# Kernel tuning notes

Hardware: AMD Instinct MI355X
Metric: run time of the kernel (lower is better)

Reference implementation:

```python
import jax, jax.numpy as jnp
import numpy as np

B, D, CIN, H, W = 2, 6, 3, 96, 96
DIM, NUM_HEADS, DEPTH = 144, 6, 2
WS = (2, 8, 8)   # window size (d, h, w)
SS = (1, 4, 4)   # shift size for odd blocks
HID = int(DIM * 2.0)
TBL = (2 * WS[0] - 1) * (2 * WS[1] - 1) * (2 * WS[2] - 1)  # 675
EPS = 1e-5


def _rpi(ws):
    # pairwise relative position index, same math as WindowAttention.get_position_index
    coords = np.stack(np.meshgrid(np.arange(ws[0]), np.arange(ws[1]), np.arange(ws[2]), indexing='ij'))
    cf = coords.reshape(3, -1).astype(np.int64)
    rc = (cf[:, :, None] - cf[:, None, :]).transpose(1, 2, 0)
    rc[..., 0] += ws[0] - 1
    rc[..., 1] += ws[1] - 1
    rc[..., 2] += ws[2] - 1
    rc[..., 0] *= (2 * ws[1] - 1) * (2 * ws[2] - 1)
    rc[..., 1] *= 2 * ws[2] - 1
    return rc.sum(-1)  # (N, N)


def _win_part_np(x, ws):
    b, d, h, w, c = x.shape
    x = x.reshape(b, d // ws[0], ws[0], h // ws[1], ws[1], w // ws[2], ws[2], c)
    return x.transpose(0, 1, 3, 5, 2, 4, 6, 7).reshape(-1, ws[0] * ws[1] * ws[2], c)


def _attn_mask(Dp, Hp, Wp, ws, ss):
    # static shift-window attention mask, same as compute_mask
    img = np.zeros((1, Dp, Hp, Wp, 1), np.float32)
    cnt = 0
    for d in (slice(-ws[0]), slice(-ws[0], -ss[0]), slice(-ss[0], None)):
        for h in (slice(-ws[1]), slice(-ws[1], -ss[1]), slice(-ss[1], None)):
            for w in (slice(-ws[2]), slice(-ws[2], -ss[2]), slice(-ss[2], None)):
                img[:, d, h, w, :] = cnt
                cnt += 1
    mw = _win_part_np(img, ws)[..., 0]  # (nW, N)
    am = mw[:, None, :] - mw[:, :, None]
    return np.where(am != 0, np.float32(-100.0), np.float32(0.0))


RPI = jnp.asarray(_rpi(WS))            # (N, N) int
MASK = jnp.asarray(_attn_mask(D, H, W, WS, SS))  # (nW, N, N)


def _ln(x, g, b):
    mu = jnp.mean(x, -1, keepdims=True)
    var = jnp.mean(jnp.square(x - mu), -1, keepdims=True)
    return (x - mu) * jax.lax.rsqrt(var + EPS) * g + b


def _win_part(x, ws):
    b, d, h, w, c = x.shape
    x = x.reshape(b, d // ws[0], ws[0], h // ws[1], ws[1], w // ws[2], ws[2], c)
    return x.transpose(0, 1, 3, 5, 2, 4, 6, 7).reshape(-1, ws[0] * ws[1] * ws[2], c)


def _win_rev(xw, ws, b, d, h, w):
    x = xw.reshape(b, d // ws[0], h // ws[1], w // ws[2], ws[0], ws[1], ws[2], -1)
    return x.transpose(0, 1, 4, 2, 5, 3, 6, 7).reshape(b, d, h, w, -1)


def _stl(x, i, shifted, params):
    # one Swin Transformer Layer; x: (B, D, H, W, C)
    n1g, n1b, qkvw, qkvb, rpb, projw, projb, n2g, n2b, fc1w, fc1b, fc2w, fc2b = params
    b, d, h, w, c = x.shape
    hd = c // NUM_HEADS
    scale = hd ** -0.5
    y = _ln(x, n1g[i], n1b[i])
    if shifted:
        y = jnp.roll(y, (-SS[0], -SS[1], -SS[2]), axis=(1, 2, 3))
    xw = _win_part(y, WS)  # (B_, N, C)
    B_, N, _ = xw.shape
    qkv = jnp.einsum('bnc,oc->bno', xw, qkvw[i]) + qkvb[i]
    qkv = qkv.reshape(B_, N, 3, NUM_HEADS, hd).transpose(2, 0, 3, 1, 4)
    q, k, v = qkv[0], qkv[1], qkv[2]
    attn = jnp.einsum('bhnd,bhmd->bhnm', q * scale, k)
    bias = rpb[i][RPI].transpose(2, 0, 1)  # (heads, N, N)
    attn = attn + bias[None]
    if shifted:
        nW = MASK.shape[0]
        attn = attn.reshape(B_ // nW, nW, NUM_HEADS, N, N) + MASK[None, :, None]
        attn = attn.reshape(B_, NUM_HEADS, N, N)
    attn = jax.nn.softmax(attn, axis=-1)
    out = jnp.einsum('bhnm,bhmd->bhnd', attn, v).transpose(0, 2, 1, 3).reshape(B_, N, c)
    out = jnp.einsum('bnc,oc->bno', out, projw[i]) + projb[i]
    y = _win_rev(out, WS, b, d, h, w)
    if shifted:
        y = jnp.roll(y, (SS[0], SS[1], SS[2]), axis=(1, 2, 3))
    x = x + y
    z = _ln(x, n2g[i], n2b[i])
    z = jnp.einsum('bdhwc,oc->bdhwo', z, fc1w[i]) + fc1b[i]
    z = jax.nn.gelu(z, approximate=False)
    z = jnp.einsum('bdhwo,co->bdhwc', z, fc2w[i]) + fc2b[i]
    return x + z


def setup_inputs() -> dict:
    key = jax.random.key(0)
    ks = jax.random.split(key, 8)
    s = 0.02
    return {
        'x': jax.random.normal(ks[0], (B, D, CIN, H, W), jnp.float32),
        'conv_w': jax.random.normal(ks[1], (DIM, CIN, 1, 3, 3), jnp.float32) * s,
        'conv_b': jnp.zeros((DIM,), jnp.float32),
        'ln0_g': jnp.ones((DIM,), jnp.float32),
        'ln0_b': jnp.zeros((DIM,), jnp.float32),
        'n1g': jnp.ones((DEPTH, DIM), jnp.float32),
        'n1b': jnp.zeros((DEPTH, DIM), jnp.float32),
        'qkvw': jax.random.normal(ks[2], (DEPTH, 3 * DIM, DIM), jnp.float32) * s,
        'qkvb': jnp.zeros((DEPTH, 3 * DIM), jnp.float32),
        'rpb': jax.random.normal(ks[3], (DEPTH, TBL, NUM_HEADS), jnp.float32) * s,
        'projw': jax.random.normal(ks[4], (DEPTH, DIM, DIM), jnp.float32) * s,
        'projb': jnp.zeros((DEPTH, DIM), jnp.float32),
        'n2g': jnp.ones((DEPTH, DIM), jnp.float32),
        'n2b': jnp.zeros((DEPTH, DIM), jnp.float32),
        'fc1w': jax.random.normal(ks[5], (DEPTH, HID, DIM), jnp.float32) * s,
        'fc1b': jnp.zeros((DEPTH, HID), jnp.float32),
        'fc2w': jax.random.normal(ks[6], (DEPTH, DIM, HID), jnp.float32) * s,
        'fc2b': jnp.zeros((DEPTH, DIM), jnp.float32),
        'lin_w': jax.random.normal(ks[7], (DIM, DIM), jnp.float32) * s,
        'lin_b': jnp.zeros((DIM,), jnp.float32),
        'ln1_g': jnp.ones((DIM,), jnp.float32),
        'ln1_b': jnp.zeros((DIM,), jnp.float32),
    }


def reference(x, conv_w, conv_b, ln0_g, ln0_b, n1g, n1b, qkvw, qkvb, rpb, projw, projb,
              n2g, n2b, fc1w, fc1b, fc2w, fc2b, lin_w, lin_b, ln1_g, ln1_b):
    # x: (n, d, c, h, w)
    y = x.transpose(0, 2, 1, 3, 4)  # n c d h w
    y = jax.lax.conv_general_dilated(
        y, conv_w, (1, 1, 1), [(0, 0), (1, 1), (1, 1)],
        dimension_numbers=('NCDHW', 'OIDHW', 'NCDHW')) + conv_b[None, :, None, None, None]
    y = y.transpose(0, 2, 3, 4, 1)  # n d h w c
    y = _ln(y, ln0_g, ln0_b)
    y = y.transpose(0, 4, 1, 2, 3)  # n c d h w
    params = (n1g, n1b, qkvw, qkvb, rpb, projw, projb, n2g, n2b, fc1w, fc1b, fc2w, fc2b)
    # RSTB (num_blocks = 1): residual group (STG of DEPTH STLs) + linear + skip
    f = y.transpose(0, 2, 3, 4, 1)  # b d h w c
    for i in range(DEPTH):
        f = _stl(f, i, i % 2 == 1, params)
    f = jnp.einsum('bdhwc,oc->bdhwo', f, lin_w) + lin_b
    y = y + f.transpose(0, 4, 1, 2, 3)
    # trailing LayerNorm and rearrange back to (n, d, c, h, w)
    out = _ln(y.transpose(0, 2, 3, 4, 1), ln1_g, ln1_b)
    return out.transpose(0, 1, 4, 2, 3)
```

## Files before the change

### kernel.cpp

```cpp
#include <hip/hip_runtime.h>
#include <math.h>

#define NTOK 110592
#define NWIN 864
#define TS   15925248

typedef unsigned short u16;
typedef unsigned int   u32;
typedef __attribute__((ext_vector_type(8))) short short8;
typedef __attribute__((ext_vector_type(4))) float float4v;

__device__ __forceinline__ float bf2f(u16 v) { return __uint_as_float(((u32)v) << 16); }
__device__ __forceinline__ u16 f2bf(float f) {
    u32 u = __float_as_uint(f);
    u32 r = u + 0x7fffu + ((u >> 16) & 1u);
    return (u16)(r >> 16);
}
__device__ __forceinline__ void unpack2(u32 u, float& lo, float& hi) {
    lo = __uint_as_float(u << 16);
    hi = __uint_as_float(u & 0xffff0000u);
}
__device__ __forceinline__ u32 pack2(float lo, float hi) {
    return (u32)f2bf(lo) | ((u32)f2bf(hi) << 16);
}
__device__ __forceinline__ float wave_sum(float v) {
    #pragma unroll
    for (int o = 32; o > 0; o >>= 1) v += __shfl_xor(v, o, 64);
    return v;
}
__device__ __forceinline__ float fexp2(float x) {
    float r;
    asm("v_exp_f32 %0, %1" : "=v"(r) : "v"(x));
    return r;
}

__device__ __forceinline__ void win_to_src(int tw, int shifted, int& sb, int& sd, int& sh, int& sw) {
    int n = tw & 127;
    int win = tw >> 7;
    int ww = win % 12;
    int wh = (win / 12) % 12;
    int rest = win / 144;
    int wd = rest % 3;
    sb = rest / 3;
    int ld = n >> 6, lh = (n >> 3) & 7, lw = n & 7;
    int dr = wd * 2 + ld, hr = wh * 8 + lh, wr = ww * 8 + lw;
    if (shifted) {
        sd = (dr + 1) % 6;
        sh = (hr + 4) % 96;
        sw = (wr + 4) % 96;
    } else {
        sd = dr; sh = hr; sw = wr;
    }
}

__device__ __forceinline__ int tok_region(int t, int wdn, int whn, int wwn) {
    int dr = wdn * 2 + (t >> 6), hr = whn * 8 + ((t >> 3) & 7), wr = wwn * 8 + (t & 7);
    int rd = (dr < 4) ? 0 : ((dr < 5) ? 1 : 2);
    int rh = (hr < 88) ? 0 : ((hr < 92) ? 1 : 2);
    int rw = (wr < 88) ? 0 : ((wr < 92) ? 1 : 2);
    return rd * 9 + rh * 3 + rw;
}

__global__ __launch_bounds__(256) void convert_weights(
    const float* __restrict__ qkvw, const float* __restrict__ projw,
    const float* __restrict__ fc1w, const float* __restrict__ fc2w,
    const float* __restrict__ linw, u16* __restrict__ wbuf,
    const float* __restrict__ rpb, float* __restrict__ bexp)
{
    int i = blockIdx.x * 256 + threadIdx.x;
    if (i < 124416) wbuf[i] = f2bf(qkvw[i]);
    else if (i < 165888) wbuf[i] = f2bf(projw[i - 124416]);
    else if (i < 248832) wbuf[i] = f2bf(fc1w[i - 165888]);
    else if (i < 331776) wbuf[i] = f2bf(fc2w[i - 248832]);
    else if (i < 352512) wbuf[i] = f2bf(linw[i - 331776]);
    else if (i < 549120) {
        int k = i - 352512;
        int n = k & 127, m = (k >> 7) & 127;
        int lh = k >> 14;
        int h = lh % 6, l = lh / 6;
        int rdi = (m >> 6) - (n >> 6) + 1;
        int rhi = ((m >> 3) & 7) - ((n >> 3) & 7) + 7;
        int rwi = (m & 7) - (n & 7) + 7;
        int bi = (rdi * 15 + rhi) * 15 + rwi;
        bexp[k] = rpb[l * 4050 + bi * 6 + h] * 1.4426950408889634f;
    }
}

__global__ __launch_bounds__(256) void conv_ln0_row(
    const float* __restrict__ x, const float* __restrict__ cw, const float* __restrict__ cb,
    const float* __restrict__ g0, const float* __restrict__ b0,
    float* __restrict__ y0)
{
    int bh = blockIdx.x;
    int h = bh % 96, bd = bh / 96;
    int b = bd / 6, d = bd - b * 6;
    __shared__ float ws[192][29];
    __shared__ float xsr[9][100];
    __shared__ float cbias[192], gg[144], bbv[144];
    int tid = threadIdx.x;

    for (int i = tid; i < 9 * 98; i += 256) {
        int row = i / 98, wx = i - row * 98;
        int ci = row / 3, kh = row - 3 * ci;
        int hh = h + kh - 1, wsrc = wx - 1;
        float v = 0.f;
        if (hh >= 0 && hh < 96 && wsrc >= 0 && wsrc < 96)
            v = x[((((size_t)b * 6 + d) * 3 + ci) * 96 + hh) * 96 + wsrc];
        xsr[row][wx] = v;
    }
    for (int i = tid; i < 192 * 27; i += 256) {
        int c = i / 27, j = i - c * 27;
        ws[c][j] = (c < 144) ? cw[c * 27 + j] : 0.f;
    }
    for (int i = tid; i < 192; i += 256) cbias[i] = (i < 144) ? cb[i] : 0.f;
    for (int i = tid; i < 144; i += 256) { gg[i] = g0[i]; bbv[i] = b0[i]; }
    __syncthreads();

    int wv = tid >> 6, lane = tid & 63;
    int p0 = wv * 24;

    float a0[24], a1[24], a2[24];
    #pragma unroll
    for (int k = 0; k < 24; k++) {
        a0[k] = cbias[lane]; a1[k] = cbias[lane + 64]; a2[k] = cbias[lane + 128];
    }

    for (int cikh = 0; cikh < 9; cikh++) {
        const float* xr = &xsr[cikh][p0];
        float xv[26];
        #pragma unroll
        for (int t = 0; t < 26; t++) xv[t] = xr[t];
        #pragma unroll
        for (int kw = 0; kw < 3; kw++) {
            int j = cikh * 3 + kw;
            float w0 = ws[lane][j], w1 = ws[lane + 64][j], w2 = ws[lane + 128][j];
            #pragma unroll
            for (int k = 0; k < 24; k++) {
                float xvv = xv[k + kw];
                a0[k] += w0 * xvv; a1[k] += w1 * xvv; a2[k] += w2 * xvv;
            }
        }
    }

    #pragma unroll
    for (int k = 0; k < 24; k++) {
        int p = p0 + k;
        float v0 = a0[k], v1 = a1[k];
        float v2m = (lane < 16) ? a2[k] : 0.f;
        float s  = wave_sum(v0 + v1 + v2m);
        float s2 = wave_sum(v0 * v0 + v1 * v1 + v2m * v2m);
        float mu = s * (1.f / 144.f);
        float rstd = rsqrtf(fmaxf(s2 * (1.f / 144.f) - mu * mu, 0.f) + 1e-5f);
        size_t o = ((size_t)bh * 96 + p) * 144;
        float r0 = (v0 - mu) * rstd * gg[lane] + bbv[lane];
        float r1 = (v1 - mu) * rstd * gg[lane + 64] + bbv[lane + 64];
        y0[o + lane] = r0;
        y0[o + lane + 64] = r1;
        if (lane < 16) {
            float r2 = (a2[k] - mu) * rstd * gg[lane + 128] + bbv[lane + 128];
            y0[o + lane + 128] = r2;
        }
    }
}

template<int AMODE, int EPI, int SHIFTED, int ADDBIAS, int KTILES>
__global__ __launch_bounds__(192) void mgemm(
    const void* __restrict__ Asrc, const u16* __restrict__ Wt, const float* __restrict__ bias,
    u16* __restrict__ outb, float* __restrict__ fres, const float* __restrict__ y0,
    const float* __restrict__ lng, const float* __restrict__ lnb,
    int a_add, int a_ld, int w_ld, int o_ld, int o_add)
{
    __shared__ u16 As[64 * 152];
    int m0 = blockIdx.y * 64, n0 = blockIdx.x * 144;
    int tid = threadIdx.x;
    int wv3 = tid / 64, lane = tid & 63;
    int mrow = lane & 15, quad = lane >> 4;
    const short8 z8 = {0, 0, 0, 0, 0, 0, 0, 0};

    float4v acc[4][3];
    #pragma unroll
    for (int i = 0; i < 4; i++)
        #pragma unroll
        for (int j = 0; j < 3; j++) acc[i][j] = (float4v){0.f, 0.f, 0.f, 0.f};

    #pragma unroll
    for (int kt = 0; kt < KTILES; kt++) {
        if (kt) __syncthreads();
        if constexpr (AMODE == 5 || AMODE == 6) {
            __shared__ float gs[144], bs[144], ps[64][6];
            for (int i = tid; i < 144; i += 192) { gs[i] = lng[i]; bs[i] = lnb[i]; }
            int r = tid / 3, p = tid - 3 * r;
            int srow;
            if constexpr (AMODE == 6) {
                int bq, dq, hq, wq;
                win_to_src(a_add + m0 + r, SHIFTED, bq, dq, hq, wq);
                srow = ((bq * 6 + dq) * 96 + hq) * 96 + wq;
            } else {
                srow = a_add + m0 + r;
            }
            const float4* s4 = (const float4*)((const float*)Asrc + (size_t)srow * 144) + p * 12;
            float4 av[12];
            float s = 0.f, s2 = 0.f;
            #pragma unroll
            for (int q = 0; q < 12; q++) {
                av[q] = s4[q];
                s  += (av[q].x + av[q].y) + (av[q].z + av[q].w);
                s2 += (av[q].x * av[q].x + av[q].y * av[q].y)
                    + (av[q].z * av[q].z + av[q].w * av[q].w);
            }
            ps[r][p] = s; ps[r][3 + p] = s2;
            __syncthreads();
            float S  = ps[r][0] + ps[r][1] + ps[r][2];
            float S2 = ps[r][3] + ps[r][4] + ps[r][5];
            float mu = S * (1.f / 144.f);
            float rstd = rsqrtf(fmaxf(S2 * (1.f / 144.f) - mu * mu, 0.f) + 1e-5f);
            #pragma unroll
            for (int q = 0; q < 12; q++) {
                int n = p * 48 + q * 4;
                *(u32*)&As[r * 152 + n]     = pack2((av[q].x - mu) * rstd * gs[n]     + bs[n],
                                                    (av[q].y - mu) * rstd * gs[n + 1] + bs[n + 1]);
                *(u32*)&As[r * 152 + n + 2] = pack2((av[q].z - mu) * rstd * gs[n + 2] + bs[n + 2],
                                                    (av[q].w - mu) * rstd * gs[n + 3] + bs[n + 3]);
            }
        } else if constexpr (AMODE == 2) {
            const u16* A = (const u16*)Asrc;
            #pragma unroll
            for (int idx = tid; idx < 1152; idx += 192) {
                int r = idx / 18, c4 = idx - r * 18;
                *(short8*)&As[r * 152 + c4 * 8] =
                    *(const short8*)&A[(size_t)(a_add + m0 + r) * a_ld + kt * 144 + c4 * 8];
            }
        } else if constexpr (AMODE == 3) {
            const u16* A = (const u16*)Asrc;
            int chtok = a_ld;
            int cc = m0 / chtok;
            int t0 = m0 - cc * chtok;
            const u16* Ac = A + (size_t)cc * chtok * 144;
            #pragma unroll
            for (int idx = tid; idx < 1152; idx += 192) {
                int r = idx / 18, c4 = idx - r * 18;
                int hh = c4 / 3, sub = c4 - hh * 3;
                *(short8*)&As[r * 152 + c4 * 8] =
                    *(const short8*)&Ac[((size_t)hh * chtok + t0 + r) * 24 + sub * 8];
            }
        } else {
            const float* A = (const float*)Asrc;
            #pragma unroll
            for (int idx = tid; idx < 2304; idx += 192) {
                int r = idx / 36, c4 = idx - r * 36;
                const float4* src4 = (const float4*)&A[(size_t)(a_add + m0 + r) * a_ld + kt * 144];
                float4 v = src4[c4];
                *(u32*)&As[r * 152 + c4 * 4]     = pack2(v.x, v.y);
                *(u32*)&As[r * 152 + c4 * 4 + 2] = pack2(v.z, v.w);
            }
        }
        __syncthreads();

        const u16* Wg = Wt + (size_t)(n0 + wv3 * 48 + mrow) * w_ld + kt * 144;

        #pragma unroll
        for (int ks = 0; ks < 4; ks++) {
            int k0 = ks * 32;
            short8 af[4], bf[3];
            #pragma unroll
            for (int i = 0; i < 4; i++)
                af[i] = *(const short8*)&As[(i * 16 + mrow) * 152 + k0 + quad * 8];
            #pragma unroll
            for (int j = 0; j < 3; j++)
                bf[j] = *(const short8*)&Wg[(size_t)j * 16 * w_ld + k0 + quad * 8];
            #pragma unroll
            for (int i = 0; i < 4; i++)
                #pragma unroll
                for (int j = 0; j < 3; j++)
                    acc[i][j] = __builtin_amdgcn_mfma_f32_16x16x32_bf16(af[i], bf[j], acc[i][j], 0, 0, 0);
        }
        {
            bool tl = (quad < 2);
            short8 af[4], bf[3];
            #pragma unroll
            for (int i = 0; i < 4; i++)
                af[i] = tl ? *(const short8*)&As[(i * 16 + mrow) * 152 + 128 + quad * 8] : z8;
            #pragma unroll
            for (int j = 0; j < 3; j++)
                bf[j] = tl ? *(const short8*)&Wg[(size_t)j * 16 * w_ld + 128 + quad * 8] : z8;
            #pragma unroll
            for (int i = 0; i < 4; i++)
                #pragma unroll
                for (int j = 0; j < 3; j++)
                    acc[i][j] = __builtin_amdgcn_mfma_f32_16x16x32_bf16(af[i], bf[j], acc[i][j], 0, 0, 0);
        }
    }

    if constexpr (EPI == 6) {
        __syncthreads();
        int slot = blockIdx.x;
        #pragma unroll
        for (int i = 0; i < 4; i++)
            #pragma unroll
            for (int reg = 0; reg < 4; reg++) {
                int ml = i * 16 + quad * 4 + reg;
                #pragma unroll
                for (int j = 0; j < 3; j++) {
                    int hn = wv3 * 48 + j * 16 + mrow;
                    float v = acc[i][j][reg];
                    if (ADDBIAS) v += bias[n0 + hn];
                    if (slot == 0) v *= 0.29448890f;
                    As[ml * 152 + hn] = f2bf(v);
                }
            }
        __syncthreads();
        int chtok = o_ld;
        u32* outw = (u32*)outb;
        for (int gi = tid; gi < 4608; gi += 192) {
            int hh = gi / 768;
            int rem = gi - hh * 768;
            int t = rem / 12, dd2 = rem - t * 12;
            outw[(size_t)slot * 72 * chtok + ((size_t)hh * chtok + m0 + t) * 12 + dd2]
                = *(const u32*)&As[t * 152 + hh * 24 + dd2 * 2];
        }
    } else {
        #pragma unroll
        for (int i = 0; i < 4; i++) {
            #pragma unroll
            for (int reg = 0; reg < 4; reg++) {
                int m = m0 + i * 16 + quad * 4 + reg;
                int orow;
                if (EPI == 2 || EPI == 5) {
                    int b, d, h, w;
                    win_to_src(m, SHIFTED, b, d, h, w);
                    orow = ((b * 6 + d) * 96 + h) * 96 + w;
                } else orow = m + o_add;
                #pragma unroll
                for (int j = 0; j < 3; j++) {
                    int n = n0 + wv3 * 48 + j * 16 + mrow;
                    float v = acc[i][j][reg];
                    if (ADDBIAS) v += bias[n];
                    if (EPI == 1) v = 0.5f * v * (1.f + erff(v * 0.70710678118f));
                    if (EPI == 2 || EPI == 3) {
                        fres[(size_t)orow * 144 + n] += v;
                    } else if (EPI == 5) {
                        fres[(size_t)orow * 144 + n] = y0[(size_t)orow * 144 + n] + v;
                    } else {
                        if (EPI == 4) v += y0[(size_t)orow * o_ld + n];
                        outb[(size_t)orow * o_ld + n] = f2bf(v);
                    }
                }
            }
        }
    }
}

template<int SHIFTED>
__global__ __launch_bounds__(256) void attn_mfma(
    const u16* __restrict__ qkv,
    const float* __restrict__ bexp,
    u16* __restrict__ tok_out,
    int win_base, int chtok)
{
    int win = blockIdx.x;
    int head = blockIdx.y;
    __shared__ __align__(16) u16 Pb[4][2048];
    __shared__ __align__(16) u16 Vt[3072];
    __shared__ float invden_s[128];
    __shared__ u32 reg_pack[32];

    int tid = threadIdx.x;
    int wv = tid >> 6, lane = tid & 63;
    int c = lane & 15, quad = lane >> 4;
    int qbase = wv * 32;
    const short8 z8 = {0, 0, 0, 0, 0, 0, 0, 0};
    const float* bh_ = bexp + head * 16384;
    const u16* qb_ = qkv + ((size_t)head * chtok + (size_t)win * 128) * 24;
    const u16* kb_ = qb_ + (size_t)144 * chtok;
    const u16* vb_ = qb_ + (size_t)288 * chtok;
    int cs = (c & 7) << 3;

    int wdn = 0, whn = 0, wwn = 0;
    if (SHIFTED) {
        int wib = (win_base + win) % 432;
        wwn = wib % 12; whn = (wib / 12) % 12; wdn = wib / 144;
    }

    if (tid < 128) {
        const u32* vsrc = (const u32*)(vb_ + (size_t)tid * 24);
        #pragma unroll
        for (int i = 0; i < 12; i++) {
            u32 u = vsrc[i];
            int d0 = 2 * i, d1 = 2 * i + 1;
            Vt[((d0 << 7) + tid) ^ ((d0 & 7) << 3)] = (u16)(u & 0xffffu);
            Vt[((d1 << 7) + tid) ^ ((d1 & 7) << 3)] = (u16)(u >> 16);
        }
    }
    if (SHIFTED && tid < 32) {
        int t0 = tid * 4;
        reg_pack[tid] = (u32)tok_region(t0, wdn, whn, wwn)
                      | ((u32)tok_region(t0 + 1, wdn, whn, wwn) << 8)
                      | ((u32)tok_region(t0 + 2, wdn, whn, wwn) << 16)
                      | ((u32)tok_region(t0 + 3, wdn, whn, wwn) << 24);
    }
    __syncthreads();

    short8 aq[2];
    #pragma unroll
    for (int i = 0; i < 2; i++) {
        aq[i] = z8;
        if (quad < 3)
            aq[i] = *(const short8*)(qb_ + (size_t)(qbase + i * 16 + c) * 24 + quad * 8);
    }

    float4 bv0[8];
    {
        const float* brow = bh_ + (qbase + c) * 128;
        #pragma unroll
        for (int j = 0; j < 8; j++)
            bv0[j] = *(const float4*)(brow + j * 16 + quad * 4);
    }

    float4v s_acc[2][8];
    #pragma unroll
    for (int i = 0; i < 2; i++)
        #pragma unroll
        for (int j = 0; j < 8; j++) s_acc[i][j] = (float4v){0.f, 0.f, 0.f, 0.f};

    #pragma unroll
    for (int j = 0; j < 8; j++) {
        short8 kf = z8;
        if (quad < 3)
            kf = *(const short8*)(kb_ + (size_t)(j * 16 + c) * 24 + quad * 8);
        s_acc[0][j] = __builtin_amdgcn_mfma_f32_16x16x32_bf16(kf, aq[0], s_acc[0][j], 0, 0, 0);
        s_acc[1][j] = __builtin_amdgcn_mfma_f32_16x16x32_bf16(kf, aq[1], s_acc[1][j], 0, 0, 0);
    }

    float4v o_acc[2][2];
    #pragma unroll
    for (int i = 0; i < 2; i++)
        #pragma unroll
        for (int jv = 0; jv < 2; jv++) o_acc[i][jv] = (float4v){0.f, 0.f, 0.f, 0.f};

    u32 myreg0 = SHIFTED ? (u32)tok_region(qbase + c, wdn, whn, wwn) : 0u;
    u32 myreg1 = SHIFTED ? (u32)tok_region(qbase + 16 + c, wdn, whn, wwn) : 0u;
    float4 bv1[8];

    {
        float den = 0.f;
        #pragma unroll
        for (int j = 0; j < 8; j++) {
            float s0 = s_acc[0][j][0] + bv0[j].x;
            float s1 = s_acc[0][j][1] + bv0[j].y;
            float s2 = s_acc[0][j][2] + bv0[j].z;
            float s3 = s_acc[0][j][3] + bv0[j].w;
            if (SHIFTED) {
                u32 rv = reg_pack[j * 4 + quad];
                s0 += ((rv & 255u) == myreg0) ? 0.f : -144.2695f;
                s1 += (((rv >> 8) & 255u) == myreg0) ? 0.f : -144.2695f;
                s2 += (((rv >> 16) & 255u) == myreg0) ? 0.f : -144.2695f;
                s3 += ((rv >> 24) == myreg0) ? 0.f : -144.2695f;
            }
            float p0 = fexp2(s0), p1 = fexp2(s1), p2 = fexp2(s2), p3 = fexp2(s3);
            den += (p0 + p1) + (p2 + p3);
            u32 w0, w1;
            asm("v_cvt_pk_bf16_f32 %0, %1, %2" : "=v"(w0) : "v"(p0), "v"(p1));
            asm("v_cvt_pk_bf16_f32 %0, %1, %2" : "=v"(w1) : "v"(p2), "v"(p3));
            uint2 wpair = make_uint2(w0, w1);
            *(uint2*)&Pb[wv][((c << 7) + j * 16 + quad * 4) ^ cs] = wpair;
        }
        den += __shfl_xor(den, 16, 64);
        den += __shfl_xor(den, 32, 64);
        if (quad == 0) invden_s[qbase + c] = 1.f / den;

        {
            const float* brow = bh_ + (qbase + 16 + c) * 128;
            #pragma unroll
            for (int j = 0; j < 8; j++)
                bv1[j] = *(const float4*)(brow + j * 16 + quad * 4);
        }

        #pragma unroll
        for (int ks = 0; ks < 4; ks++) {
            short8 pf  = *(const short8*)&Pb[wv][((c << 7) + ks * 32 + quad * 8) ^ cs];
            short8 vf0 = *(const short8*)&Vt[((c << 7) + ks * 32 + quad * 8) ^ cs];
            short8 vf1 = (c < 8) ? *(const short8*)&Vt[(((16 + c) << 7) + ks * 32 + quad * 8) ^ cs] : z8;
            o_acc[0][0] = __builtin_amdgcn_mfma_f32_16x16x32_bf16(pf, vf0, o_acc[0][0], 0, 0, 0);
            o_acc[0][1] = __builtin_amdgcn_mfma_f32_16x16x32_bf16(pf, vf1, o_acc[0][1], 0, 0, 0);
        }
    }

    {
        float den = 0.f;
        #pragma unroll
        for (int j = 0; j < 8; j++) {
            float s0 = s_acc[1][j][0] + bv1[j].x;
            float s1 = s_acc[1][j][1] + bv1[j].y;
            float s2 = s_acc[1][j][2] + bv1[j].z;
            float s3 = s_acc[1][j][3] + bv1[j].w;
            if (SHIFTED) {
                u32 rv = reg_pack[j * 4 + quad];
                s0 += ((rv & 255u) == myreg1) ? 0.f : -144.2695f;
                s1 += (((rv >> 8) & 255u) == myreg1) ? 0.f : -144.2695f;
                s2 += (((rv >> 16) & 255u) == myreg1) ? 0.f : -144.2695f;
                s3 += ((rv >> 24) == myreg1) ? 0.f : -144.2695f;
            }
            float p0 = fexp2(s0), p1 = fexp2(s1), p2 = fexp2(s2), p3 = fexp2(s3);
            den += (p0 + p1) + (p2 + p3);
            u32 w0, w1;
            asm("v_cvt_pk_bf16_f32 %0, %1, %2" : "=v"(w0) : "v"(p0), "v"(p1));
            asm("v_cvt_pk_bf16_f32 %0, %1, %2" : "=v"(w1) : "v"(p2), "v"(p3));
            uint2 wpair = make_uint2(w0, w1);
            *(uint2*)&Pb[wv][((c << 7) + j * 16 + quad * 4) ^ cs] = wpair;
        }
        den += __shfl_xor(den, 16, 64);
        den += __shfl_xor(den, 32, 64);
        if (quad == 0) invden_s[qbase + 16 + c] = 1.f / den;

        #pragma unroll
        for (int ks = 0; ks < 4; ks++) {
            short8 pf  = *(const short8*)&Pb[wv][((c << 7) + ks * 32 + quad * 8) ^ cs];
            short8 vf0 = *(const short8*)&Vt[((c << 7) + ks * 32 + quad * 8) ^ cs];
            short8 vf1 = (c < 8) ? *(const short8*)&Vt[(((16 + c) << 7) + ks * 32 + quad * 8) ^ cs] : z8;
            o_acc[1][0] = __builtin_amdgcn_mfma_f32_16x16x32_bf16(pf, vf0, o_acc[1][0], 0, 0, 0);
            o_acc[1][1] = __builtin_amdgcn_mfma_f32_16x16x32_bf16(pf, vf1, o_acc[1][1], 0, 0, 0);
        }
    }

    float* ob = (float*)&Pb[wv][0];
    #pragma unroll
    for (int i = 0; i < 2; i++)
        #pragma unroll
        for (int jv = 0; jv < 2; jv++) {
            int d = jv * 16 + c;
            if (d < 24) {
                #pragma unroll
                for (int r = 0; r < 4; r++)
                    ob[(i * 16 + quad * 4 + r) * 26 + d] = o_acc[i][jv][r];
            }
        }
    __syncthreads();

    if (tid < 128) {
        const float2* ol = (const float2*)((const float*)&Pb[0][0]
                                           + (tid >> 5) * 1024 + (tid & 31) * 26);
        float inv = invden_s[tid];
        u32* orow = (u32*)tok_out + ((size_t)head * chtok + (size_t)win * 128 + tid) * 12;
        #pragma unroll
        for (int d2 = 0; d2 < 12; d2++) {
            float2 v = ol[d2];
            orow[d2] = pack2(v.x * inv, v.y * inv);
        }
    }
}

__global__ __launch_bounds__(256) void final_ln_out_kernel(
    const u16* __restrict__ gsrc, const float* __restrict__ g, const float* __restrict__ bt,
    float* __restrict__ out)
{
    int bh = blockIdx.x;
    int h = bh % 96, d = (bh / 96) % 6, b = bh / 576;
    __shared__ u16 tile[96][152];
    __shared__ float stat[96][2];
    const u16* src = gsrc + (size_t)bh * 96 * 144;
    for (int i = threadIdx.x; i < 1728; i += 256) {
        int wt = i / 18, c8 = i - wt * 18;
        *(short8*)&tile[wt][c8 * 8] = *(const short8*)&src[wt * 144 + c8 * 8];
    }
    __syncthreads();
    if (threadIdx.x < 96) {
        const u32* row = (const u32*)&tile[threadIdx.x][0];
        float s = 0.f, s2 = 0.f;
        #pragma unroll
        for (int j = 0; j < 72; j++) {
            float lo, hi; unpack2(row[j], lo, hi);
            s += lo + hi; s2 += lo * lo + hi * hi;
        }
        float mu = s * (1.f / 144.f);
        float var = s2 * (1.f / 144.f) - mu * mu;
        stat[threadIdx.x][0] = mu;
        stat[threadIdx.x][1] = rsqrtf(fmaxf(var, 0.f) + 1e-5f);
    }
    __syncthreads();
    size_t obase = ((size_t)(b * 6 + d) * 144) * 9216 + h * 96;
    for (int i = threadIdx.x; i < 96 * 144; i += blockDim.x) {
        int c = i / 96, wt = i - c * 96;
        out[obase + (size_t)c * 9216 + wt] =
            (bf2f(tile[wt][c]) - stat[wt][0]) * stat[wt][1] * g[c] + bt[c];
    }
}

extern "C" void kernel_launch(void* const* d_in, const int* in_sizes, int n_in,
                              void* d_out, int out_size, void* d_ws, size_t ws_size,
                              hipStream_t stream) {
    const float* x     = (const float*)d_in[0];
    const float* convw = (const float*)d_in[1];
    const float* convb = (const float*)d_in[2];
    const float* ln0g  = (const float*)d_in[3];
    const float* ln0b  = (const float*)d_in[4];
    const float* n1g   = (const float*)d_in[5];
    const float* n1b   = (const float*)d_in[6];
    const float* qkvw  = (const float*)d_in[7];
    const float* qkvb  = (const float*)d_in[8];
    const float* rpb   = (const float*)d_in[9];
    const float* projw = (const float*)d_in[10];
    const float* projb = (const float*)d_in[11];
    const float* n2g   = (const float*)d_in[12];
    const float* n2b   = (const float*)d_in[13];
    const float* fc1w  = (const float*)d_in[14];
    const float* fc1b  = (const float*)d_in[15];
    const float* fc2w  = (const float*)d_in[16];
    const float* fc2b  = (const float*)d_in[17];
    const float* linw  = (const float*)d_in[18];
    const float* linb  = (const float*)d_in[19];
    const float* ln1g  = (const float*)d_in[20];
    const float* ln1b  = (const float*)d_in[21];

    char* wp = (char*)d_ws;
    float* f    = (float*)wp;             wp += (size_t)TS * 4;
    u16*   tok  = (u16*)wp;               wp += (size_t)TS * 2;
    u16*   wbuf = (u16*)wp;               wp += 352512ull * 2;
    float* bexp = (float*)wp;             wp += 196608ull * 4;
    u16*   qkvbuf = (u16*)wp;
    size_t rest = ws_size - (size_t)(wp - (char*)d_ws);
    int nch = (rest >= (size_t)NTOK * 432 * 2) ? 1
            : (rest >= (size_t)NTOK * 216 * 2) ? 2 : 4;
    int nm  = (rest >= (size_t)NTOK * 288 * 2) ? 1
            : (rest >= (size_t)NTOK * 144 * 2) ? 2 : 3;
    float* y0 = (float*)d_out;

    convert_weights<<<2145, 256, 0, stream>>>(qkvw, projw, fc1w, fc2w, linw, wbuf, rpb, bexp);
    conv_ln0_row<<<1152, 256, 0, stream>>>(x, convw, convb, ln0g, ln0b, y0);

    for (int layer = 0; layer < 2; ++layer) {
        const u16* qw  = wbuf + (size_t)layer * 62208;
        const u16* pw  = wbuf + 124416 + (size_t)layer * 20736;
        const u16* f1w = wbuf + 165888 + (size_t)layer * 41472;
        const u16* f2w = wbuf + 248832 + (size_t)layer * 41472;
        const float* qb  = qkvb + (size_t)layer * 432;
        const float* pb  = projb + (size_t)layer * 144;
        const float* g1  = n1g + layer * 144;
        const float* b1  = n1b + layer * 144;
        const float* g2  = n2g + layer * 144;
        const float* b2  = n2b + layer * 144;
        const float* f1b = fc1b + (size_t)layer * 288;
        const float* f2b = fc2b + (size_t)layer * 144;
        const float* bx  = bexp + (size_t)layer * 98304;

        const float* asrc = (layer == 0) ? y0 : f;
        int chtok = NTOK / nch, chwin = NWIN / nch;
        for (int c = 0; c < nch; c++) {
            if (layer == 0)
                mgemm<6, 6, 0, 1, 1><<<dim3(3, chtok / 64), 192, 0, stream>>>(
                    asrc, qw, qb, qkvbuf, nullptr, nullptr, g1, b1,
                    c * chtok, 144, 144, chtok, 0);
            else
                mgemm<6, 6, 1, 1, 1><<<dim3(3, chtok / 64), 192, 0, stream>>>(
                    asrc, qw, qb, qkvbuf, nullptr, nullptr, g1, b1,
                    c * chtok, 144, 144, chtok, 0);
            u16* ob = tok + (size_t)c * chtok * 144;
            if (layer == 0)
                attn_mfma<0><<<dim3(chwin, 6), 256, 0, stream>>>(qkvbuf, bx, ob, c * chwin, chtok);
            else
                attn_mfma<1><<<dim3(chwin, 6), 256, 0, stream>>>(qkvbuf, bx, ob, c * chwin, chtok);
        }

        if (layer == 0)
            mgemm<3, 5, 0, 1, 1><<<dim3(1, NTOK / 64), 192, 0, stream>>>(
                tok, pw, pb, nullptr, f, y0, nullptr, nullptr, 0, chtok, 144, 144, 0);
        else
            mgemm<3, 2, 1, 1, 1><<<dim3(1, NTOK / 64), 192, 0, stream>>>(
                tok, pw, pb, nullptr, f, nullptr, nullptr, nullptr, 0, chtok, 144, 144, 0);

        int fcch = NTOK / nm;
        for (int c = 0; c < nm; c++) {
            int mst = c * fcch;
            mgemm<5, 1, 0, 1, 1><<<dim3(2, fcch / 64), 192, 0, stream>>>(
                f, f1w, f1b, qkvbuf, nullptr, nullptr, g2, b2, mst, 144, 144, 288, 0);
            mgemm<2, 3, 0, 1, 2><<<dim3(1, fcch / 64), 192, 0, stream>>>(
                qkvbuf, f2w, f2b, nullptr, f, nullptr, nullptr, nullptr, 0, 288, 288, 144, mst);
        }
    }

    mgemm<0, 4, 0, 1, 1><<<dim3(1, NTOK / 64), 192, 0, stream>>>(
        f, wbuf + 331776, linb, tok, nullptr, y0, nullptr, nullptr, 0, 144, 144, 144, 0);

    final_ln_out_kernel<<<2 * 6 * 96, 256, 0, stream>>>(tok, ln1g, ln1b, (float*)d_out);
}
```

Before: 754.4 us.

## Split attention across 8 waves with 16 query rows each

The window attention kernel now launches 512 threads (8 waves) per window-head block, and each wave handles 16 query rows instead of 32. This halves per-wave register use and the serial per-wave work, and spreads the final output store over all threads. In exchange, K fragments and bias loads are fetched by twice as many waves, the P staging buffer in shared memory doubles, and larger blocks may limit how many blocks fit per CU.

```diff
diff --git a/kernel.cpp b/kernel.cpp
--- a/kernel.cpp
+++ b/kernel.cpp
@@ -351,7 +351,7 @@
 }
 
 template<int SHIFTED>
-__global__ __launch_bounds__(256) void attn_mfma(
+__global__ __launch_bounds__(512) void attn_mfma(
     const u16* __restrict__ qkv,
     const float* __restrict__ bexp,
     u16* __restrict__ tok_out,
@@ -359,7 +359,7 @@
 {
     int win = blockIdx.x;
     int head = blockIdx.y;
-    __shared__ __align__(16) u16 Pb[4][2048];
+    __shared__ __align__(16) u16 Pb[8][2048];
     __shared__ __align__(16) u16 Vt[3072];
     __shared__ float invden_s[128];
     __shared__ u32 reg_pack[32];
@@ -367,7 +367,7 @@
     int tid = threadIdx.x;
     int wv = tid >> 6, lane = tid & 63;
     int c = lane & 15, quad = lane >> 4;
-    int qbase = wv * 32;
+    int qbase = wv * 16;
     const short8 z8 = {0, 0, 0, 0, 0, 0, 0, 0};
     const float* bh_ = bexp + head * 16384;
     const u16* qb_ = qkv + ((size_t)head * chtok + (size_t)win * 128) * 24;
@@ -400,152 +400,90 @@
     }
     __syncthreads();
 
-    short8 aq[2];
-    #pragma unroll
-    for (int i = 0; i < 2; i++) {
-        aq[i] = z8;
-        if (quad < 3)
-            aq[i] = *(const short8*)(qb_ + (size_t)(qbase + i * 16 + c) * 24 + quad * 8);
-    }
-
-    float4 bv0[8];
+    short8 aq = z8;
+    if (quad < 3)
+        aq = *(const short8*)(qb_ + (size_t)(qbase + c) * 24 + quad * 8);
+
+    float4 bv[8];
     {
         const float* brow = bh_ + (qbase + c) * 128;
         #pragma unroll
         for (int j = 0; j < 8; j++)
-            bv0[j] = *(const float4*)(brow + j * 16 + quad * 4);
-    }
-
-    float4v s_acc[2][8];
-    #pragma unroll
-    for (int i = 0; i < 2; i++)
-        #pragma unroll
-        for (int j = 0; j < 8; j++) s_acc[i][j] = (float4v){0.f, 0.f, 0.f, 0.f};
+            bv[j] = *(const float4*)(brow + j * 16 + quad * 4);
+    }
+
+    float4v s_acc[8];
+    #pragma unroll
+    for (int j = 0; j < 8; j++) s_acc[j] = (float4v){0.f, 0.f, 0.f, 0.f};
 
     #pragma unroll
     for (int j = 0; j < 8; j++) {
         short8 kf = z8;
         if (quad < 3)
             kf = *(const short8*)(kb_ + (size_t)(j * 16 + c) * 24 + quad * 8);
-        s_acc[0][j] = __builtin_amdgcn_mfma_f32_16x16x32_bf16(kf, aq[0], s_acc[0][j], 0, 0, 0);
-        s_acc[1][j] = __builtin_amdgcn_mfma_f32_16x16x32_bf16(kf, aq[1], s_acc[1][j], 0, 0, 0);
-    }
-
-    float4v o_acc[2][2];
-    #pragma unroll
-    for (int i = 0; i < 2; i++)
-        #pragma unroll
-        for (int jv = 0; jv < 2; jv++) o_acc[i][jv] = (float4v){0.f, 0.f, 0.f, 0.f};
-
-    u32 myreg0 = SHIFTED ? (u32)tok_region(qbase + c, wdn, whn, wwn) : 0u;
-    u32 myreg1 = SHIFTED ? (u32)tok_region(qbase + 16 + c, wdn, whn, wwn) : 0u;
-    float4 bv1[8];
-
-    {
-        float den = 0.f;
-        #pragma unroll
-        for (int j = 0; j < 8; j++) {
-            float s0 = s_acc[0][j][0] + bv0[j].x;
-            float s1 = s_acc[0][j][1] + bv0[j].y;
-            float s2 = s_acc[0][j][2] + bv0[j].z;
-            float s3 = s_acc[0][j][3] + bv0[j].w;
-            if (SHIFTED) {
-                u32 rv = reg_pack[j * 4 + quad];
-                s0 += ((rv & 255u) == myreg0) ? 0.f : -144.2695f;
-                s1 += (((rv >> 8) & 255u) == myreg0) ? 0.f : -144.2695f;
-                s2 += (((rv >> 16) & 255u) == myreg0) ? 0.f : -144.2695f;
-                s3 += ((rv >> 24) == myreg0) ? 0.f : -144.2695f;
-            }
-            float p0 = fexp2(s0), p1 = fexp2(s1), p2 = fexp2(s2), p3 = fexp2(s3);
-            den += (p0 + p1) + (p2 + p3);
-            u32 w0, w1;
-            asm("v_cvt_pk_bf16_f32 %0, %1, %2" : "=v"(w0) : "v"(p0), "v"(p1));
-            asm("v_cvt_pk_bf16_f32 %0, %1, %2" : "=v"(w1) : "v"(p2), "v"(p3));
-            uint2 wpair = make_uint2(w0, w1);
-            *(uint2*)&Pb[wv][((c << 7) + j * 16 + quad * 4) ^ cs] = wpair;
-        }
-        den += __shfl_xor(den, 16, 64);
-        den += __shfl_xor(den, 32, 64);
-        if (quad == 0) invden_s[qbase + c] = 1.f / den;
-
-        {
-            const float* brow = bh_ + (qbase + 16 + c) * 128;
-            #pragma unroll
-            for (int j = 0; j < 8; j++)
-                bv1[j] = *(const float4*)(brow + j * 16 + quad * 4);
-        }
-
-        #pragma unroll
-        for (int ks = 0; ks < 4; ks++) {
-            short8 pf  = *(const short8*)&Pb[wv][((c << 7) + ks * 32 + quad * 8) ^ cs];
-            short8 vf0 = *(const short8*)&Vt[((c << 7) + ks * 32 + quad * 8) ^ cs];
-            short8 vf1 = (c < 8) ? *(const short8*)&Vt[(((16 + c) << 7) + ks * 32 + quad * 8) ^ cs] : z8;
-            o_acc[0][0] = __builtin_amdgcn_mfma_f32_16x16x32_bf16(pf, vf0, o_acc[0][0], 0, 0, 0);
-            o_acc[0][1] = __builtin_amdgcn_mfma_f32_16x16x32_bf16(pf, vf1, o_acc[0][1], 0, 0, 0);
-        }
-    }
-
-    {
-        float den = 0.f;
-        #pragma unroll
-        for (int j = 0; j < 8; j++) {
-            float s0 = s_acc[1][j][0] + bv1[j].x;
-            float s1 = s_acc[1][j][1] + bv1[j].y;
-            float s2 = s_acc[1][j][2] + bv1[j].z;
-            float s3 = s_acc[1][j][3] + bv1[j].w;
-            if (SHIFTED) {
-                u32 rv = reg_pack[j * 4 + quad];
-                s0 += ((rv & 255u) == myreg1) ? 0.f : -144.2695f;
-                s1 += (((rv >> 8) & 255u) == myreg1) ? 0.f : -144.2695f;
-                s2 += (((rv >> 16) & 255u) == myreg1) ? 0.f : -144.2695f;
-                s3 += ((rv >> 24) == myreg1) ? 0.f : -144.2695f;
-            }
-            float p0 = fexp2(s0), p1 = fexp2(s1), p2 = fexp2(s2), p3 = fexp2(s3);
-            den += (p0 + p1) + (p2 + p3);
-            u32 w0, w1;
-            asm("v_cvt_pk_bf16_f32 %0, %1, %2" : "=v"(w0) : "v"(p0), "v"(p1));
-            asm("v_cvt_pk_bf16_f32 %0, %1, %2" : "=v"(w1) : "v"(p2), "v"(p3));
-            uint2 wpair = make_uint2(w0, w1);
-            *(uint2*)&Pb[wv][((c << 7) + j * 16 + quad * 4) ^ cs] = wpair;
-        }
-        den += __shfl_xor(den, 16, 64);
-        den += __shfl_xor(den, 32, 64);
-        if (quad == 0) invden_s[qbase + 16 + c] = 1.f / den;
-
-        #pragma unroll
-        for (int ks = 0; ks < 4; ks++) {
-            short8 pf  = *(const short8*)&Pb[wv][((c << 7) + ks * 32 + quad * 8) ^ cs];
-            short8 vf0 = *(const short8*)&Vt[((c << 7) + ks * 32 + quad * 8) ^ cs];
-            short8 vf1 = (c < 8) ? *(const short8*)&Vt[(((16 + c) << 7) + ks * 32 + quad * 8) ^ cs] : z8;
-            o_acc[1][0] = __builtin_amdgcn_mfma_f32_16x16x32_bf16(pf, vf0, o_acc[1][0], 0, 0, 0);
-            o_acc[1][1] = __builtin_amdgcn_mfma_f32_16x16x32_bf16(pf, vf1, o_acc[1][1], 0, 0, 0);
-        }
+        s_acc[j] = __builtin_amdgcn_mfma_f32_16x16x32_bf16(kf, aq, s_acc[j], 0, 0, 0);
+    }
+
+    u32 myreg = SHIFTED ? (u32)tok_region(qbase + c, wdn, whn, wwn) : 0u;
+
+    float den = 0.f;
+    #pragma unroll
+    for (int j = 0; j < 8; j++) {
+        float s0 = s_acc[j][0] + bv[j].x;
+        float s1 = s_acc[j][1] + bv[j].y;
+        float s2 = s_acc[j][2] + bv[j].z;
+        float s3 = s_acc[j][3] + bv[j].w;
+        if (SHIFTED) {
+            u32 rv = reg_pack[j * 4 + quad];
+            s0 += ((rv & 255u) == myreg) ? 0.f : -144.2695f;
+            s1 += (((rv >> 8) & 255u) == myreg) ? 0.f : -144.2695f;
+            s2 += (((rv >> 16) & 255u) == myreg) ? 0.f : -144.2695f;
+            s3 += ((rv >> 24) == myreg) ? 0.f : -144.2695f;
+        }
+        float p0 = fexp2(s0), p1 = fexp2(s1), p2 = fexp2(s2), p3 = fexp2(s3);
+        den += (p0 + p1) + (p2 + p3);
+        u32 w0, w1;
+        asm("v_cvt_pk_bf16_f32 %0, %1, %2" : "=v"(w0) : "v"(p0), "v"(p1));
+        asm("v_cvt_pk_bf16_f32 %0, %1, %2" : "=v"(w1) : "v"(p2), "v"(p3));
+        uint2 wpair = make_uint2(w0, w1);
+        *(uint2*)&Pb[wv][((c << 7) + j * 16 + quad * 4) ^ cs] = wpair;
+    }
+    den += __shfl_xor(den, 16, 64);
+    den += __shfl_xor(den, 32, 64);
+    if (quad == 0) invden_s[qbase + c] = 1.f / den;
+
+    float4v o_acc[2];
+    o_acc[0] = (float4v){0.f, 0.f, 0.f, 0.f};
+    o_acc[1] = (float4v){0.f, 0.f, 0.f, 0.f};
+
+    #pragma unroll
+    for (int ks = 0; ks < 4; ks++) {
+        short8 pf  = *(const short8*)&Pb[wv][((c << 7) + ks * 32 + quad * 8) ^ cs];
+        short8 vf0 = *(const short8*)&Vt[((c << 7) + ks * 32 + quad * 8) ^ cs];
+        short8 vf1 = (c < 8) ? *(const short8*)&Vt[(((16 + c) << 7) + ks * 32 + quad * 8) ^ cs] : z8;
+        o_acc[0] = __builtin_amdgcn_mfma_f32_16x16x32_bf16(pf, vf0, o_acc[0], 0, 0, 0);
+        o_acc[1] = __builtin_amdgcn_mfma_f32_16x16x32_bf16(pf, vf1, o_acc[1], 0, 0, 0);
     }
 
     float* ob = (float*)&Pb[wv][0];
     #pragma unroll
-    for (int i = 0; i < 2; i++)
-        #pragma unroll
-        for (int jv = 0; jv < 2; jv++) {
-            int d = jv * 16 + c;
-            if (d < 24) {
-                #pragma unroll
-                for (int r = 0; r < 4; r++)
-                    ob[(i * 16 + quad * 4 + r) * 26 + d] = o_acc[i][jv][r];
-            }
-        }
+    for (int jv = 0; jv < 2; jv++) {
+        int d = jv * 16 + c;
+        if (d < 24) {
+            #pragma unroll
+            for (int r = 0; r < 4; r++)
+                ob[(quad * 4 + r) * 26 + d] = o_acc[jv][r];
+        }
+    }
     __syncthreads();
 
-    if (tid < 128) {
-        const float2* ol = (const float2*)((const float*)&Pb[0][0]
-                                           + (tid >> 5) * 1024 + (tid & 31) * 26);
-        float inv = invden_s[tid];
-        u32* orow = (u32*)tok_out + ((size_t)head * chtok + (size_t)win * 128 + tid) * 12;
-        #pragma unroll
-        for (int d2 = 0; d2 < 12; d2++) {
-            float2 v = ol[d2];
-            orow[d2] = pack2(v.x * inv, v.y * inv);
-        }
+    for (int gi = tid; gi < 1536; gi += 512) {
+        int row = gi / 12, d2 = gi - row * 12;
+        const float2* ol = (const float2*)((const float*)&Pb[row >> 4][0] + (row & 15) * 26);
+        float2 v = ol[d2];
+        float inv = invden_s[row];
+        u32* orow = (u32*)tok_out + ((size_t)head * chtok + (size_t)win * 128 + row) * 12;
+        orow[d2] = pack2(v.x * inv, v.y * inv);
     }
 }
 
@@ -655,9 +593,9 @@
                     c * chtok, 144, 144, chtok, 0);
             u16* ob = tok + (size_t)c * chtok * 144;
             if (layer == 0)
-                attn_mfma<0><<<dim3(chwin, 6), 256, 0, stream>>>(qkvbuf, bx, ob, c * chwin, chtok);
+                attn_mfma<0><<<dim3(chwin, 6), 512, 0, stream>>>(qkvbuf, bx, ob, c * chwin, chtok);
             else
-                attn_mfma<1><<<dim3(chwin, 6), 256, 0, stream>>>(qkvbuf, bx, ob, c * chwin, chtok);
+                attn_mfma<1><<<dim3(chwin, 6), 512, 0, stream>>>(qkvbuf, bx, ob, c * chwin, chtok);
         }
 
         if (layer == 0)
```

After: 785.1 us. 1.04x slower.
